# Kernel tuning notes

Hardware: AMD Instinct MI355X
Metric: run time of the kernel (lower is better)

The kernel has to match this reference:

```python
import jax, jax.numpy as jnp
import numpy as np

EPS = 1e-5
NUM_GROUPS = 32
NUM_HEADS = 4


def setup_inputs() -> dict:
    key = jax.random.key(0)
    ks = jax.random.split(key, 3)
    B, C, H, W = 4, 256, 64, 64
    x = jax.random.normal(ks[0], (B, C, H, W), dtype=jnp.float32)
    gn_w = jnp.ones((C,), jnp.float32)
    gn_b = jnp.zeros((C,), jnp.float32)
    qkv_w = jax.random.normal(ks[1], (3 * C, C), dtype=jnp.float32) * (C ** -0.5)
    qkv_b = jnp.zeros((3 * C,), jnp.float32)
    proj_w = jax.random.normal(ks[2], (C, C), dtype=jnp.float32) * (C ** -0.5)
    proj_b = jnp.zeros((C,), jnp.float32)
    return {"x": x, "gn_w": gn_w, "gn_b": gn_b, "qkv_w": qkv_w,
            "qkv_b": qkv_b, "proj_w": proj_w, "proj_b": proj_b}


def _group_norm(x, w, b):
    B, C, H, W = x.shape
    xg = x.reshape(B, NUM_GROUPS, C // NUM_GROUPS, H, W)
    mean = xg.mean(axis=(2, 3, 4), keepdims=True)
    var = xg.var(axis=(2, 3, 4), keepdims=True)
    xn = ((xg - mean) * jax.lax.rsqrt(var + EPS)).reshape(B, C, H, W)
    return xn * w[None, :, None, None] + b[None, :, None, None]


def reference(x, gn_w, gn_b, qkv_w, qkv_b, proj_w, proj_b):
    B, C, H, W = x.shape
    nh = NUM_HEADS
    d = C // nh
    L = H * W
    h = _group_norm(x, gn_w, gn_b)
    # 1x1 conv == channel matmul
    qkv = jnp.einsum('oc,bchw->bohw', qkv_w, h) + qkv_b[None, :, None, None]
    q, k, v = jnp.split(qkv, 3, axis=1)
    # (B, C, H, W) -> (B, nh, L, d)
    def to_heads(t):
        return t.reshape(B, nh, d, L).transpose(0, 1, 3, 2)
    q, k, v = to_heads(q), to_heads(k), to_heads(v)
    scale = d ** -0.5
    attn = jax.nn.softmax(jnp.einsum('bhqd,bhkd->bhqk', q, k) * scale, axis=-1)
    o = jnp.einsum('bhqk,bhkd->bhqd', attn, v)          # (B, nh, L, d)
    o = o.transpose(0, 1, 3, 2).reshape(B, C, H, W)
    o = jnp.einsum('oc,bchw->bohw', proj_w, o) + proj_b[None, :, None, None]
    return x + o
```

## Files before the change

### kernel.cpp

```cpp
#include <hip/hip_runtime.h>

#define B_   4
#define C_   256
#define L_   4096
#define NH_  4
#define D_   64
#define G_   32
#define CPG_ 8

typedef __bf16 bf16x8 __attribute__((ext_vector_type(8)));
typedef float  f32x4  __attribute__((ext_vector_type(4)));

__device__ __forceinline__ ushort f2bf(float f) {
  union { float f; unsigned u; } c; c.f = f;
  unsigned u = c.u;
  return (ushort)((u + 0x7fffu + ((u >> 16) & 1u)) >> 16);
}
__device__ __forceinline__ float bf2f(ushort h) {
  union { unsigned u; float f; } c; c.u = ((unsigned)h) << 16; return c.f;
}
__device__ __forceinline__ unsigned fbits(float f) {
  union { float f; unsigned u; } c; c.f = f; return c.u;
}
__device__ __forceinline__ float fastexp2(float x) {
#if __has_builtin(__builtin_amdgcn_exp2f)
  return __builtin_amdgcn_exp2f(x);
#else
  return exp2f(x);
#endif
}

__global__ __launch_bounds__(256) void pre_kernel(const float* __restrict__ x,
                                                  const float* __restrict__ wqf,
                                                  const float* __restrict__ wpf,
                                                  ushort* __restrict__ wq,
                                                  ushort* __restrict__ wp,
                                                  float* __restrict__ stats2) {
  int bidx = blockIdx.x;
  int tid  = threadIdx.x;
  if (bidx >= 1024) {
    int t = (bidx - 1024) * 256 + tid;
    const int NQ4 = (768 * 256) / 4;
    float4 v;
    if (t < NQ4) {
      v = ((const float4*)wqf)[t];
      ((ushort4*)wq)[t] = make_ushort4(f2bf(v.x), f2bf(v.y), f2bf(v.z), f2bf(v.w));
    } else {
      int i = t - NQ4;
      v = ((const float4*)wpf)[i];
      ((ushort4*)wp)[i] = make_ushort4(f2bf(v.x), f2bf(v.y), f2bf(v.z), f2bf(v.w));
    }
    return;
  }
  int bg = bidx >> 3, chunk = bidx & 7;
  int b = bg >> 5, g = bg & 31;
  const float* xg = x + ((size_t)b * C_ + g * CPG_) * L_ + chunk * 512;

  float s = 0.f, ss = 0.f;
  for (int c = 0; c < CPG_; ++c) {
    float2 v = ((const float2*)(xg + (size_t)c * L_))[tid];
    s  += v.x + v.y;
    ss += v.x * v.x + v.y * v.y;
  }
  for (int off = 32; off; off >>= 1) { s += __shfl_xor(s, off); ss += __shfl_xor(ss, off); }
  __shared__ float red[8];
  int w = tid >> 6;
  if ((tid & 63) == 0) { red[w] = s; red[4 + w] = ss; }
  __syncthreads();
  if (tid == 0) {
    stats2[bidx * 2]     = red[0] + red[1] + red[2] + red[3];
    stats2[bidx * 2 + 1] = red[4] + red[5] + red[6] + red[7];
  }
}

__global__ __launch_bounds__(256) void gn_apply(const float* __restrict__ x,
                                                const float* __restrict__ gw,
                                                const float* __restrict__ gb,
                                                const float* __restrict__ stats2,
                                                ushort* __restrict__ hT) {
  int bg = blockIdx.x >> 3, chunk = blockIdx.x & 7;
  int b = bg >> 5, g = bg & 31;
  const float* xg = x + ((size_t)b * C_ + g * CPG_) * L_;
  int tid = threadIdx.x;

  float s = 0.f, ss = 0.f;
#pragma unroll
  for (int c2 = 0; c2 < 8; ++c2) {
    s  += stats2[(bg * 8 + c2) * 2];
    ss += stats2[(bg * 8 + c2) * 2 + 1];
  }
  const float inv_n = 1.0f / (CPG_ * L_);
  float mean = s * inv_n;
  float var  = ss * inv_n - mean * mean;
  float rstd = rsqrtf(var + 1e-5f);

  float wv[CPG_], bv[CPG_];
  for (int c = 0; c < CPG_; ++c) { wv[c] = gw[g * CPG_ + c]; bv[c] = gb[g * CPG_ + c]; }

  for (int li = 0; li < 2; ++li) {
    int l = chunk * 512 + li * 256 + tid;
    union { ushort s[8]; uint4 u; } o;
    for (int c = 0; c < CPG_; ++c) {
      float v = xg[(size_t)c * L_ + l];
      o.s[c] = f2bf((v - mean) * rstd * wv[c] + bv[c]);
    }
    *(uint4*)(hT + ((size_t)b * L_ + l) * C_ + g * CPG_) = o.u;
  }
}

__global__ __launch_bounds__(256) void qkv_kernel(const ushort* __restrict__ hT,
                                                  const ushort* __restrict__ w,
                                                  const float* __restrict__ bias,
                                                  ushort* __restrict__ q,
                                                  ushort* __restrict__ k,
                                                  ushort* __restrict__ v) {
  int wid  = blockIdx.x * 4 + (threadIdx.x >> 6);
  int lane = threadIdx.x & 63;
  int quad = lane >> 4, col = lane & 15;
  int ot   = wid % 12;
  int rest = wid / 12;
  int lt   = rest & 127;
  int b    = rest >> 7;
  int o0 = ot * 64, l0 = lt * 32;

  const ushort* abase = w  + (size_t)(o0 + col) * C_ + quad * 8;
  const ushort* bbase = hT + ((size_t)b * L_ + l0 + col) * C_ + quad * 8;

  f32x4 acc[4][2];
  for (int i = 0; i < 4; ++i) for (int j = 0; j < 2; ++j)
    acc[i][j] = (f32x4){0.f, 0.f, 0.f, 0.f};

#pragma unroll
  for (int k0 = 0; k0 < C_; k0 += 32) {
    bf16x8 a[4], bb[2];
#pragma unroll
    for (int i = 0; i < 4; ++i) a[i]  = *(const bf16x8*)(abase + (size_t)(i * 16) * C_ + k0);
#pragma unroll
    for (int j = 0; j < 2; ++j) bb[j] = *(const bf16x8*)(bbase + (size_t)(j * 16) * C_ + k0);
#pragma unroll
    for (int i = 0; i < 4; ++i)
#pragma unroll
      for (int j = 0; j < 2; ++j)
        acc[i][j] = __builtin_amdgcn_mfma_f32_16x16x32_bf16(a[i], bb[j], acc[i][j], 0, 0, 0);
  }

  int third = o0 >> 8;
  int hh    = (o0 & 255) >> 6;
  float scale = (third == 0) ? 0.180336880111120f : 1.0f;
#pragma unroll
  for (int i = 0; i < 4; ++i) {
    int oo = o0 + i * 16 + quad * 4;
    int dd = i * 16 + quad * 4;
#pragma unroll
    for (int j = 0; j < 2; ++j) {
      int l = l0 + j * 16 + col;
      ushort pk[4];
      for (int r = 0; r < 4; ++r) pk[r] = f2bf((acc[i][j][r] + bias[oo + r]) * scale);
      if (third < 2) {
        ushort* dst = (third ? k : q) + (((size_t)(b * NH_ + hh) * L_ + l) * D_ + dd);
        *(ushort4*)dst = make_ushort4(pk[0], pk[1], pk[2], pk[3]);
      } else {
        for (int r = 0; r < 4; ++r)
          v[((size_t)(b * NH_ + hh) * D_ + dd + r) * L_ + l] = pk[r];
      }
    }
  }
}

__global__ __launch_bounds__(256, 2) void attn_kernel(const ushort* __restrict__ q,
                                                      const ushort* __restrict__ k,
                                                      const ushort* __restrict__ v,
                                                      ushort* __restrict__ p0,
                                                      ushort* __restrict__ p1,
                                                      float* __restrict__ psumbuf) {
  __shared__ __align__(16) ushort k_lds[2][64][72];
  __shared__ __align__(16) ushort v_lds[2][64][72];

  int tid   = threadIdx.x;
  int w     = tid >> 6, lane = tid & 63;
  int quad  = lane >> 4, col = lane & 15;
  int bid   = (int)blockIdx.x;
  bid = (bid & 7) * 64 + (bid >> 3);
  int split = bid >> 8;
  int bh    = (bid >> 4) & 15;
  int qblk  = bid & 15;

  const ushort* qp = q + (size_t)bh * L_ * D_;
  const ushort* kp = k + (size_t)bh * L_ * D_;
  const ushort* vp = v + (size_t)bh * D_ * L_;

  int qrow0 = qblk * 256 + w * 64;
  bf16x8 bq[4][2];
#pragma unroll
  for (int f = 0; f < 4; ++f)
#pragma unroll
    for (int c = 0; c < 2; ++c)
      bq[f][c] = *(const bf16x8*)(qp + (size_t)(qrow0 + f * 16 + col) * D_ + c * 32 + quad * 8);

  f32x4 oacc[4][4];
#pragma unroll
  for (int f = 0; f < 4; ++f)
    for (int t = 0; t < 4; ++t) oacc[f][t] = (f32x4){0.f, 0.f, 0.f, 0.f};
  f32x4 pacc[4];
#pragma unroll
  for (int f = 0; f < 4; ++f) pacc[f] = (f32x4){0.f, 0.f, 0.f, 0.f};
  const f32x4 Z = (f32x4){0.f, 0.f, 0.f, 0.f};

  union { ushort s[8]; bf16x8 v8; } one_u;
#pragma unroll
  for (int i = 0; i < 8; ++i) one_u.s[i] = 0x3F80;
  bf16x8 ones = one_u.v8;

  int vrow = tid >> 2, vchunk = tid & 3;
  int vwoff = (vchunk >> 1) * 32 + (vchunk & 1) * 4;
  int kt0 = split * (L_ / 2), kt_end = kt0 + L_ / 2;

  {
    const uint4* ksrc = (const uint4*)(kp + (size_t)kt0 * D_);
    uint4 a  = ksrc[tid];
    uint4 b2 = ksrc[tid + 256];
    const uint4* vsrc = (const uint4*)(vp + (size_t)vrow * L_ + kt0);
    uint4 c0 = vsrc[vchunk * 2];
    uint4 c1 = vsrc[vchunk * 2 + 1];
    *(uint4*)&k_lds[0][tid >> 3][(tid & 7) * 8] = a;
    *(uint4*)&k_lds[0][32 + (tid >> 3)][(tid & 7) * 8] = b2;
    ushort* vb = &v_lds[0][vrow][vwoff];
    *(uint2*)(vb + 0)  = make_uint2(c0.x, c0.y);
    *(uint2*)(vb + 8)  = make_uint2(c0.z, c0.w);
    *(uint2*)(vb + 16) = make_uint2(c1.x, c1.y);
    *(uint2*)(vb + 24) = make_uint2(c1.z, c1.w);
  }
  __syncthreads();

  int cur = 0;
  for (int kt = kt0; kt < kt_end; kt += 64) {
    bool has_next = (kt + 64) < kt_end;

    f32x4 s[2][4][2];
#pragma unroll
    for (int h = 0; h < 2; ++h) {
      bf16x8 a00 = *(const bf16x8*)&k_lds[cur][h * 32 + col][quad * 8];
      bf16x8 a01 = *(const bf16x8*)&k_lds[cur][h * 32 + col][32 + quad * 8];
      bf16x8 a10 = *(const bf16x8*)&k_lds[cur][h * 32 + 16 + col][quad * 8];
      bf16x8 a11 = *(const bf16x8*)&k_lds[cur][h * 32 + 16 + col][32 + quad * 8];
#pragma unroll
      for (int f = 0; f < 4; ++f) {
        s[h][f][0] = __builtin_amdgcn_mfma_f32_16x16x32_bf16(a00, bq[f][0], Z, 0, 0, 0);
        s[h][f][1] = __builtin_amdgcn_mfma_f32_16x16x32_bf16(a10, bq[f][0], Z, 0, 0, 0);
        s[h][f][0] = __builtin_amdgcn_mfma_f32_16x16x32_bf16(a01, bq[f][1], s[h][f][0], 0, 0, 0);
        s[h][f][1] = __builtin_amdgcn_mfma_f32_16x16x32_bf16(a11, bq[f][1], s[h][f][1], 0, 0, 0);
      }
    }

    uint4 nk0, nk1, nv0, nv1;
    if (has_next) {
      const uint4* ksrc = (const uint4*)(kp + (size_t)(kt + 64) * D_);
      nk0 = ksrc[tid];
      nk1 = ksrc[tid + 256];
      const uint4* vsrc = (const uint4*)(vp + (size_t)vrow * L_ + (kt + 64));
      nv0 = vsrc[vchunk * 2];
      nv1 = vsrc[vchunk * 2 + 1];
    }

#pragma unroll
    for (int h = 0; h < 2; ++h) {
      bf16x8 pb[4];
#pragma unroll
      for (int f = 0; f < 4; ++f) {
        float pe0[4], pe1[4];
#pragma unroll
        for (int r = 0; r < 4; ++r) {
          pe0[r] = fastexp2(s[h][f][0][r]);
          pe1[r] = fastexp2(s[h][f][1][r]);
        }
        union { unsigned u[4]; bf16x8 v8; } pc;
        pc.u[0] = __builtin_amdgcn_perm(fbits(pe0[1]), fbits(pe0[0]), 0x07060302u);
        pc.u[1] = __builtin_amdgcn_perm(fbits(pe0[3]), fbits(pe0[2]), 0x07060302u);
        pc.u[2] = __builtin_amdgcn_perm(fbits(pe1[1]), fbits(pe1[0]), 0x07060302u);
        pc.u[3] = __builtin_amdgcn_perm(fbits(pe1[3]), fbits(pe1[2]), 0x07060302u);
        pb[f] = pc.v8;
      }
#pragma unroll
      for (int f = 0; f < 4; ++f)
        pacc[f] = __builtin_amdgcn_mfma_f32_16x16x32_bf16(ones, pb[f], pacc[f], 0, 0, 0);
#pragma unroll
      for (int t = 0; t < 4; ++t) {
        bf16x8 av = *(const bf16x8*)&v_lds[cur][t * 16 + col][h * 32 + quad * 8];
#pragma unroll
        for (int f = 0; f < 4; ++f)
          oacc[f][t] = __builtin_amdgcn_mfma_f32_16x16x32_bf16(av, pb[f], oacc[f][t], 0, 0, 0);
      }
    }

    if (has_next) {
      int nb = cur ^ 1;
      *(uint4*)&k_lds[nb][tid >> 3][(tid & 7) * 8] = nk0;
      *(uint4*)&k_lds[nb][32 + (tid >> 3)][(tid & 7) * 8] = nk1;
      ushort* vb = &v_lds[nb][vrow][vwoff];
      *(uint2*)(vb + 0)  = make_uint2(nv0.x, nv0.y);
      *(uint2*)(vb + 8)  = make_uint2(nv0.z, nv0.w);
      *(uint2*)(vb + 16) = make_uint2(nv1.x, nv1.y);
      *(uint2*)(vb + 24) = make_uint2(nv1.z, nv1.w);
      __syncthreads();
      cur = nb;
    }
  }

  ushort* po = split ? p1 : p0;
#pragma unroll
  for (int f = 0; f < 4; ++f) {
    for (int t = 0; t < 4; ++t) {
      ushort ok[4];
      for (int r = 0; r < 4; ++r) ok[r] = f2bf(oacc[f][t][r]);
      ushort* dst = po + ((size_t)bh * L_ + qrow0 + f * 16 + col) * D_ + t * 16 + quad * 4;
      *(ushort4*)dst = make_ushort4(ok[0], ok[1], ok[2], ok[3]);
    }
    if (quad == 0)
      psumbuf[split * (16 * L_) + bh * L_ + qrow0 + f * 16 + col] = pacc[f][0];
  }
}

__global__ __launch_bounds__(256) void comb_kernel(ushort* __restrict__ p0,
                                                   const ushort* __restrict__ p1,
                                                   const float* __restrict__ ps) {
  int idx = blockIdx.x * 256 + threadIdx.x;
  int row = idx >> 3;
  float inv = 1.0f / (ps[row] + ps[16 * L_ + row]);
  union { uint4 u; ushort s[8]; } ua, ub, o;
  ua.u = ((const uint4*)p0)[idx];
  ub.u = ((const uint4*)p1)[idx];
#pragma unroll
  for (int e = 0; e < 8; ++e)
    o.s[e] = f2bf((bf2f(ua.s[e]) + bf2f(ub.s[e])) * inv);
  ((uint4*)p0)[idx] = o.u;
}

template<bool FUSED>
__global__ __launch_bounds__(256) void proj_kernel(const ushort* __restrict__ p0,
                                                   const ushort* __restrict__ p1,
                                                   const float* __restrict__ ps,
                                                   const ushort* __restrict__ pw,
                                                   const float* __restrict__ pb,
                                                   const float* __restrict__ x,
                                                   float* __restrict__ out) {
  int wid  = blockIdx.x * 4 + (threadIdx.x >> 6);
  int lane = threadIdx.x & 63;
  int quad = lane >> 4, col = lane & 15;
  int oct  = wid & 7;
  int rest = wid >> 3;
  int lt   = rest & 127;
  int b    = rest >> 7;
  int l0 = lt * 32, oc0 = oct * 32;

  float inv[4][2];
  if (FUSED) {
#pragma unroll
    for (int hh = 0; hh < 4; ++hh)
#pragma unroll
      for (int i = 0; i < 2; ++i) {
        size_t row = (size_t)(b * NH_ + hh) * L_ + (l0 + i * 16 + col);
        inv[hh][i] = 1.0f / (ps[row] + ps[16 * L_ + row]);
      }
  }

  f32x4 acc[2][2];
  for (int i = 0; i < 2; ++i) for (int j = 0; j < 2; ++j)
    acc[i][j] = (f32x4){0.f, 0.f, 0.f, 0.f};

#pragma unroll
  for (int k0 = 0; k0 < C_; k0 += 32) {
    int hh = k0 >> 6, dk = k0 & 63;
    bf16x8 a[2], bb[2];
#pragma unroll
    for (int i = 0; i < 2; ++i) {
      size_t off = ((size_t)(b * NH_ + hh) * L_ + l0 + i * 16 + col) * D_ + dk + quad * 8;
      if (FUSED) {
        union { uint4 u; ushort s[8]; } ua, ub;
        union { ushort s[8]; bf16x8 v; } oa;
        ua.u = *(const uint4*)(p0 + off);
        ub.u = *(const uint4*)(p1 + off);
#pragma unroll
        for (int e = 0; e < 8; ++e)
          oa.s[e] = f2bf((bf2f(ua.s[e]) + bf2f(ub.s[e])) * inv[hh][i]);
        a[i] = oa.v;
      } else {
        a[i] = *(const bf16x8*)(p0 + off);
      }
    }
#pragma unroll
    for (int j = 0; j < 2; ++j)
      bb[j] = *(const bf16x8*)(pw + (size_t)(oc0 + j * 16 + col) * C_ + k0 + quad * 8);
#pragma unroll
    for (int i = 0; i < 2; ++i)
#pragma unroll
      for (int j = 0; j < 2; ++j)
        acc[i][j] = __builtin_amdgcn_mfma_f32_16x16x32_bf16(a[i], bb[j], acc[i][j], 0, 0, 0);
  }

#pragma unroll
  for (int j = 0; j < 2; ++j) {
    int oc = oc0 + j * 16 + col;
    float bias = pb[oc];
#pragma unroll
    for (int i = 0; i < 2; ++i) {
      int l = l0 + i * 16 + quad * 4;
      size_t off = ((size_t)b * C_ + oc) * L_ + l;
      float4 xv = *(const float4*)(x + off);
      float4 ov = make_float4(acc[i][j][0] + bias + xv.x,
                              acc[i][j][1] + bias + xv.y,
                              acc[i][j][2] + bias + xv.z,
                              acc[i][j][3] + bias + xv.w);
      *(float4*)(out + off) = ov;
    }
  }
}

extern "C" void kernel_launch(void* const* d_in, const int* in_sizes, int n_in,
                              void* d_out, int out_size, void* d_ws, size_t ws_size,
                              hipStream_t stream) {
  const float* x      = (const float*)d_in[0];
  const float* gn_w   = (const float*)d_in[1];
  const float* gn_b   = (const float*)d_in[2];
  const float* qkv_w  = (const float*)d_in[3];
  const float* qkv_b  = (const float*)d_in[4];
  const float* proj_w = (const float*)d_in[5];
  const float* proj_b = (const float*)d_in[6];
  float* out = (float*)d_out;

  const size_t TEN = (size_t)B_ * C_ * L_;
  ushort* ws  = (ushort*)d_ws;
  ushort* q   = ws;
  ushort* k   = ws + TEN;
  ushort* v   = ws + 2 * TEN;
  ushort* oat = ws + 3 * TEN;
  ushort* wq  = ws + 4 * TEN;
  ushort* wp  = wq + 768 * 256;
  ushort* wend = wp + 256 * 256;
  ushort* hT  = (ushort*)d_out;
  float*  st2 = (float*)((ushort*)d_out + TEN);

  const size_t base_bytes  = (size_t)(wend - ws) * 2;
  const size_t need_fused  = base_bytes + TEN * 2  + (size_t)2 * 16 * L_ * 4 ;
  const bool   fused       = ws_size >= need_fused;

  pre_kernel <<<1280,      256, 0, stream>>>(x, qkv_w, proj_w, wq, wp, st2);
  gn_apply   <<<1024,      256, 0, stream>>>(x, gn_w, gn_b, st2, hT);
  qkv_kernel <<<6144 / 4,  256, 0, stream>>>(hT, wq, qkv_b, q, k, v);

  if (fused) {
    ushort* p1w = wend;
    float*  psw = (float*)(wend + TEN);
    attn_kernel<<<512, 256, 0, stream>>>(q, k, v, oat, p1w, psw);
    proj_kernel<true><<<4096 / 4, 256, 0, stream>>>(oat, p1w, psw, wp, proj_b, x, out);
  } else {
    ushort* p1d = (ushort*)d_out + TEN;
    float*  psb = (float*)d_out;
    attn_kernel<<<512, 256, 0, stream>>>(q, k, v, oat, p1d, psb);
    comb_kernel<<<2048, 256, 0, stream>>>(oat, p1d, psb);
    proj_kernel<false><<<4096 / 4, 256, 0, stream>>>(oat, oat, psb, wp, proj_b, x, out);
  }
}
```

Before: 214.1 us.

## Stage combined attention output in LDS for proj and widen gn_apply stores

The fused proj kernel now has each block combine the two attention partials and their softmax normalisation once into a shared LDS tile. Its four waves read that tile, where before each wave redid the loads and combine for the same 32 rows across eight output-channel tiles. Block indexing is remapped so a block's waves share an L tile and split output channels. gn_apply now handles 32 channels (four groups) per thread, writing 64 contiguous bytes per row instead of 16, with half the blocks. The cost is LDS use, a barrier in proj, and more registers per thread in gn_apply.

```diff
diff --git a/kernel.cpp b/kernel.cpp
--- a/kernel.cpp
+++ b/kernel.cpp
@@ -78,34 +78,42 @@
                                                 const float* __restrict__ gb,
                                                 const float* __restrict__ stats2,
                                                 ushort* __restrict__ hT) {
-  int bg = blockIdx.x >> 3, chunk = blockIdx.x & 7;
-  int b = bg >> 5, g = bg & 31;
-  const float* xg = x + ((size_t)b * C_ + g * CPG_) * L_;
+  int bid = blockIdx.x;
+  int b     = bid >> 7;
+  int lslab = (bid & 127) >> 3;
+  int cslab = bid & 7;
   int tid = threadIdx.x;
-
-  float s = 0.f, ss = 0.f;
-#pragma unroll
-  for (int c2 = 0; c2 < 8; ++c2) {
-    s  += stats2[(bg * 8 + c2) * 2];
-    ss += stats2[(bg * 8 + c2) * 2 + 1];
-  }
+  int l0 = lslab * 256, c0 = cslab * 32;
+
   const float inv_n = 1.0f / (CPG_ * L_);
-  float mean = s * inv_n;
-  float var  = ss * inv_n - mean * mean;
-  float rstd = rsqrtf(var + 1e-5f);
-
-  float wv[CPG_], bv[CPG_];
-  for (int c = 0; c < CPG_; ++c) { wv[c] = gw[g * CPG_ + c]; bv[c] = gb[g * CPG_ + c]; }
-
-  for (int li = 0; li < 2; ++li) {
-    int l = chunk * 512 + li * 256 + tid;
-    union { ushort s[8]; uint4 u; } o;
-    for (int c = 0; c < CPG_; ++c) {
-      float v = xg[(size_t)c * L_ + l];
-      o.s[c] = f2bf((v - mean) * rstd * wv[c] + bv[c]);
-    }
-    *(uint4*)(hT + ((size_t)b * L_ + l) * C_ + g * CPG_) = o.u;
-  }
+  float mean[4], rstd[4];
+#pragma unroll
+  for (int gg = 0; gg < 4; ++gg) {
+    int bg = b * 32 + cslab * 4 + gg;
+    float s = 0.f, ss = 0.f;
+#pragma unroll
+    for (int c2 = 0; c2 < 8; ++c2) {
+      s  += stats2[(bg * 8 + c2) * 2];
+      ss += stats2[(bg * 8 + c2) * 2 + 1];
+    }
+    mean[gg] = s * inv_n;
+    float var = ss * inv_n - mean[gg] * mean[gg];
+    rstd[gg] = rsqrtf(var + 1e-5f);
+  }
+
+  int l = l0 + tid;
+  union { uint4 u[4]; ushort s[32]; } o;
+#pragma unroll
+  for (int c = 0; c < 32; ++c) {
+    int gg = c >> 3;
+    float wv = gw[c0 + c], bv = gb[c0 + c];
+    float v = x[((size_t)b * C_ + c0 + c) * L_ + l];
+    o.s[c] = f2bf((v - mean[gg]) * rstd[gg] * wv + bv);
+  }
+  ushort* dst = hT + ((size_t)b * L_ + l) * C_ + c0;
+#pragma unroll
+  for (int i = 0; i < 4; ++i)
+    ((uint4*)dst)[i] = o.u[i];
 }
 
 __global__ __launch_bounds__(256) void qkv_kernel(const ushort* __restrict__ hT,
@@ -343,24 +351,34 @@
                                                    const float* __restrict__ pb,
                                                    const float* __restrict__ x,
                                                    float* __restrict__ out) {
-  int wid  = blockIdx.x * 4 + (threadIdx.x >> 6);
-  int lane = threadIdx.x & 63;
+  __shared__ __align__(16) ushort a_lds[32][264];
+
+  int tid  = threadIdx.x;
+  int w    = tid >> 6, lane = tid & 63;
   int quad = lane >> 4, col = lane & 15;
-  int oct  = wid & 7;
-  int rest = wid >> 3;
-  int lt   = rest & 127;
-  int b    = rest >> 7;
+  int bid  = (int)blockIdx.x;
+  int oct  = (bid & 1) * 4 + w;
+  int lt   = (bid >> 1) & 127;
+  int b    = bid >> 8;
   int l0 = lt * 32, oc0 = oct * 32;
 
-  float inv[4][2];
   if (FUSED) {
-#pragma unroll
-    for (int hh = 0; hh < 4; ++hh)
-#pragma unroll
-      for (int i = 0; i < 2; ++i) {
-        size_t row = (size_t)(b * NH_ + hh) * L_ + (l0 + i * 16 + col);
-        inv[hh][i] = 1.0f / (ps[row] + ps[16 * L_ + row]);
-      }
+    int ll = tid & 31, chunk = tid >> 5;
+    int hh = chunk >> 1, d0 = (chunk & 1) * 32;
+    size_t row = (size_t)(b * NH_ + hh) * L_ + l0 + ll;
+    float inv = 1.0f / (ps[row] + ps[16 * L_ + row]);
+    const uint4* s0 = (const uint4*)(p0 + row * D_ + d0);
+    const uint4* s1 = (const uint4*)(p1 + row * D_ + d0);
+    union { uint4 u[4]; ushort s[32]; } ua, ub, o;
+#pragma unroll
+    for (int i = 0; i < 4; ++i) { ua.u[i] = s0[i]; ub.u[i] = s1[i]; }
+#pragma unroll
+    for (int e = 0; e < 32; ++e)
+      o.s[e] = f2bf((bf2f(ua.s[e]) + bf2f(ub.s[e])) * inv);
+#pragma unroll
+    for (int i = 0; i < 4; ++i)
+      *(uint4*)&a_lds[ll][chunk * 32 + i * 8] = o.u[i];
+    __syncthreads();
   }
 
   f32x4 acc[2][2];
@@ -373,18 +391,10 @@
     bf16x8 a[2], bb[2];
 #pragma unroll
     for (int i = 0; i < 2; ++i) {
-      size_t off = ((size_t)(b * NH_ + hh) * L_ + l0 + i * 16 + col) * D_ + dk + quad * 8;
       if (FUSED) {
-        union { uint4 u; ushort s[8]; } ua, ub;
-        union { ushort s[8]; bf16x8 v; } oa;
-        ua.u = *(const uint4*)(p0 + off);
-        ub.u = *(const uint4*)(p1 + off);
-#pragma unroll
-        for (int e = 0; e < 8; ++e)
-          oa.s[e] = f2bf((bf2f(ua.s[e]) + bf2f(ub.s[e])) * inv[hh][i]);
-        a[i] = oa.v;
+        a[i] = *(const bf16x8*)&a_lds[i * 16 + col][k0 + quad * 8];
       } else {
-        a[i] = *(const bf16x8*)(p0 + off);
+        a[i] = *(const bf16x8*)(p0 + ((size_t)(b * NH_ + hh) * L_ + l0 + i * 16 + col) * D_ + dk + quad * 8);
       }
     }
 #pragma unroll
@@ -444,19 +454,19 @@
   const bool   fused       = ws_size >= need_fused;
 
   pre_kernel <<<1280,      256, 0, stream>>>(x, qkv_w, proj_w, wq, wp, st2);
-  gn_apply   <<<1024,      256, 0, stream>>>(x, gn_w, gn_b, st2, hT);
+  gn_apply   <<<512,       256, 0, stream>>>(x, gn_w, gn_b, st2, hT);
   qkv_kernel <<<6144 / 4,  256, 0, stream>>>(hT, wq, qkv_b, q, k, v);
 
   if (fused) {
     ushort* p1w = wend;
     float*  psw = (float*)(wend + TEN);
     attn_kernel<<<512, 256, 0, stream>>>(q, k, v, oat, p1w, psw);
-    proj_kernel<true><<<4096 / 4, 256, 0, stream>>>(oat, p1w, psw, wp, proj_b, x, out);
+    proj_kernel<true><<<1024, 256, 0, stream>>>(oat, p1w, psw, wp, proj_b, x, out);
   } else {
     ushort* p1d = (ushort*)d_out + TEN;
     float*  psb = (float*)d_out;
     attn_kernel<<<512, 256, 0, stream>>>(q, k, v, oat, p1d, psb);
     comb_kernel<<<2048, 256, 0, stream>>>(oat, p1d, psb);
-    proj_kernel<false><<<4096 / 4, 256, 0, stream>>>(oat, oat, psb, wp, proj_b, x, out);
-  }
-}
+    proj_kernel<false><<<1024, 256, 0, stream>>>(oat, oat, psb, wp, proj_b, x, out);
+  }
+}
```

Result: faster. 206.4 us (-3.6%).
